# Optimization experiments

Measured on AMD Instinct MI355X. Metric: run time of the kernel, lower is better.

The kernel has to match this reference:

```python
import jax, jax.numpy as jnp
import numpy as np

N_NODES = 50000
N_EDGES = 600000
IN_DIM = 128
HID = 128
OUT_DIM = 40
NUM_REL = 3
LN_EPS = 1e-5


def layer_norm(x, g, b):
    mu = jnp.mean(x, axis=-1, keepdims=True)
    var = jnp.var(x, axis=-1, keepdims=True)
    return (x - mu) * jax.lax.rsqrt(var + LN_EPS) * g + b


def rgcn_conv(x, edge_index, edge_type, w_rel, w_root, bias, aggr):
    """PyG-style RGCNConv: out = x @ W_root + bias + sum_r aggr_r(x_src @ W_r)."""
    src, dst = edge_index[0], edge_index[1]
    out = x @ w_root + bias                      # [N, F_out]
    for r in range(NUM_REL):                     # small fixed relation loop
        h = x @ w_rel[r]                         # transform-then-gather: [N, F_out]
        msg = h[src]                             # [E, F_out]
        mask = (edge_type == r)[:, None]
        if aggr == 'add':
            msg = jnp.where(mask, msg, 0.0)
            agg = jax.ops.segment_sum(msg, dst, num_segments=N_NODES)
        else:  # 'max'; empty segments -> 0 (matches PyG scatter_reduce include_self=False over zeros)
            msg = jnp.where(mask, msg, -jnp.inf)
            agg = jax.ops.segment_max(msg, dst, num_segments=N_NODES)
            agg = jnp.where(jnp.isfinite(agg), agg, 0.0)
        out = out + agg
    return out


def setup_inputs() -> dict:
    key = jax.random.key(0)
    ks = jax.random.split(key, 16)
    f32 = jnp.float32
    def lin(k, fan_in, shape):
        return jax.random.normal(k, shape, dtype=f32) / np.sqrt(fan_in)
    inp = {
        'x': jax.random.normal(ks[0], (N_NODES, IN_DIM), dtype=f32),
        'edge_index': jax.random.randint(ks[1], (2, N_EDGES), 0, N_NODES),
        'edge_type': jax.random.randint(ks[2], (N_EDGES,), 0, NUM_REL),
        # conv1
        'w1_rel': lin(ks[3], IN_DIM, (NUM_REL, IN_DIM, HID)),
        'w1_root': lin(ks[4], IN_DIM, (IN_DIM, HID)),
        'b1': jnp.zeros((HID,), f32),
        'ln1_g': jnp.ones((HID,), f32), 'ln1_b': jnp.zeros((HID,), f32),
        # conv2
        'w2_rel': lin(ks[5], HID, (NUM_REL, HID, HID)),
        'w2_root': lin(ks[6], HID, (HID, HID)),
        'b2': jnp.zeros((HID,), f32),
        'ln2_g': jnp.ones((HID,), f32), 'ln2_b': jnp.zeros((HID,), f32),
        # classifier
        'cw1': lin(ks[7], HID, (HID, HID)), 'cb1': jnp.zeros((HID,), f32),
        'cln1_g': jnp.ones((HID,), f32), 'cln1_b': jnp.zeros((HID,), f32),
        'cw2': lin(ks[8], HID, (HID, HID // 2)), 'cb2': jnp.zeros((HID // 2,), f32),
        'cln2_g': jnp.ones((HID // 2,), f32), 'cln2_b': jnp.zeros((HID // 2,), f32),
        'cw3': lin(ks[9], HID // 2, (HID // 2, OUT_DIM)), 'cb3': jnp.zeros((OUT_DIM,), f32),
    }
    return inp


def reference(x, edge_index, edge_type,
              w1_rel, w1_root, b1, ln1_g, ln1_b,
              w2_rel, w2_root, b2, ln2_g, ln2_b,
              cw1, cb1, cln1_g, cln1_b,
              cw2, cb2, cln2_g, cln2_b,
              cw3, cb3):
    # eval mode: edge dropout and feature dropout are identity
    h = rgcn_conv(x, edge_index, edge_type, w1_rel, w1_root, b1, 'add')
    h = jax.nn.relu(layer_norm(h, ln1_g, ln1_b))
    x1 = h
    h = rgcn_conv(x1, edge_index, edge_type, w2_rel, w2_root, b2, 'max')
    h = jax.nn.relu(layer_norm(h, ln2_g, ln2_b))
    h = h + x1 * 0.2
    # classifier MLP
    h = jax.nn.gelu(layer_norm(h @ cw1 + cb1, cln1_g, cln1_b), approximate=False)
    h = jax.nn.gelu(layer_norm(h @ cw2 + cb2, cln2_g, cln2_b), approximate=False)
    h = h @ cw3 + cb3
    return jax.nn.log_softmax(h, axis=1)
```

## Files before the change

kernel.cpp:

```cpp
#include <hip/hip_runtime.h>
#include <hip/hip_bf16.h>
#include <math.h>


typedef __attribute__((ext_vector_type(8))) short bf16x8;
typedef __attribute__((ext_vector_type(4))) float f32x4;
typedef unsigned short ushort_t;

__device__ __forceinline__ ushort_t bf16rne(float v) {
    unsigned u = __float_as_uint(v);
    return (ushort_t)((u + 0x7FFFu + ((u >> 16) & 1u)) >> 16);
}

__device__ __forceinline__ void split_bf16(float v, ushort_t& h, ushort_t& l) {
    ushort_t hu = bf16rne(v);
    float hf = __uint_as_float((unsigned)hu << 16);
    h = hu;
    l = bf16rne(v - hf);
}

__device__ __forceinline__ float bf2f(unsigned u16) {
    return __uint_as_float(u16 << 16);
}

__device__ __forceinline__ float4 unpack_bf4(uint2 u) {
    return make_float4(bf2f(u.x & 0xFFFFu), bf2f(u.x >> 16),
                       bf2f(u.y & 0xFFFFu), bf2f(u.y >> 16));
}

__device__ __forceinline__ float2 unpack_bf2(unsigned u) {
    return make_float2(__uint_as_float(u << 16),
                       __uint_as_float(u & 0xFFFF0000u));
}

__device__ __forceinline__ uint2 pack_bf4(float4 v) {
    uint2 o;
    o.x = (unsigned)bf16rne(v.x) | ((unsigned)bf16rne(v.y) << 16);
    o.y = (unsigned)bf16rne(v.z) | ((unsigned)bf16rne(v.w) << 16);
    return o;
}

__device__ __forceinline__ unsigned pack_bf2(float2 v) {
    return (unsigned)bf16rne(v.x) | ((unsigned)bf16rne(v.y) << 16);
}

__device__ __forceinline__ void conv_body128(const float* __restrict__ W,
                                             ushort_t* __restrict__ out,
                                             int idx) {
    constexpr int NCF = 8;
    constexpr size_t PST = (size_t)4 * NCF * 512;
    int l = idx & 63;
    int cf = (idx >> 6) & 7;
    int ks = idx >> 9;
    int col = cf * 16 + (l & 15);
    int k0 = ks * 32 + (l >> 4) * 8;
    size_t base = (((size_t)ks * NCF + cf) * 64 + l) * 8;
#pragma unroll
    for (int j = 0; j < 8; ++j) {
        ushort_t h, lo_;
        split_bf16(W[(size_t)(k0 + j) * 128 + col], h, lo_);
        out[base + j] = h;
        out[PST + base + j] = lo_;
    }
}

__global__ __launch_bounds__(256) void convert_all_x2bf(
    const float* __restrict__ w1_root, const float* __restrict__ w1_rel,
    const float* __restrict__ w2_root, const float* __restrict__ w2_rel,
    const float* __restrict__ cw1, const float* __restrict__ cw2,
    ushort_t* __restrict__ wfb,
    const float* __restrict__ x, ushort_t* __restrict__ xh, int n4) {
    int b = blockIdx.x;
    if (b >= 76) {
        int g = (b - 76) * 256 + threadIdx.x;
        if (g < n4) {
            float4 v = ((const float4*)x)[g];
            ((uint2*)xh)[g] = pack_bf4(v);
        }
        return;
    }
    if (b < 72) {
        const float* src;
        int slot;
        if (b < 8)       { slot = 0;              src = w1_root; }
        else if (b < 32) { int r = (b - 8) >> 3;  slot = 1 + r; src = w1_rel + (size_t)r * 16384; }
        else if (b < 40) { slot = 4;              src = w2_root; }
        else if (b < 64) { int r = (b - 40) >> 3; slot = 5 + r; src = w2_rel + (size_t)r * 16384; }
        else             { slot = 8;              src = cw1; }
        int lb = (b < 8) ? b : (b < 32) ? ((b - 8) & 7) : (b < 40) ? (b - 32)
               : (b < 64) ? ((b - 40) & 7) : (b - 64);
        conv_body128(src, wfb + (size_t)slot * 32768, lb * 256 + threadIdx.x);
    } else {
        constexpr int NCF = 4;
        constexpr size_t PST = (size_t)4 * NCF * 512;
        int idx = (b - 72) * 256 + threadIdx.x;
        ushort_t* out = wfb + (size_t)9 * 32768;
        int l = idx & 63;
        int cf = (idx >> 6) & 3;
        int ks = idx >> 8;
        int col = cf * 16 + (l & 15);
        int k0 = ks * 32 + (l >> 4) * 8;
        size_t base = (((size_t)ks * NCF + cf) * 64 + l) * 8;
#pragma unroll
        for (int j = 0; j < 8; ++j) {
            ushort_t h, lo_;
            split_bf16(cw2[(size_t)(k0 + j) * 64 + col], h, lo_);
            out[base + j] = h;
            out[PST + base + j] = lo_;
        }
    }
}

template <int NCOL, int NSEG, int FUSE>
__global__ __launch_bounds__(256, 3) void gemm_bf(
    const ushort_t* __restrict__ A0, const ushort_t* __restrict__ A1,
    const ushort_t* __restrict__ A2, const ushort_t* __restrict__ A3,
    const ushort_t* __restrict__ wfrag, const float* __restrict__ bias,
    const float* __restrict__ lng, const float* __restrict__ lnb,
    void* __restrict__ Yv, int M) {
    constexpr int NCF = NCOL / 16;
    constexpr int WF = NCOL / 32;
    constexpr int PST = 4 * NCF * 512;
    constexpr int WSEG = 2 * PST;
    constexpr int RS = NCOL * 4 + 16;
    constexpr int EPB = 64 * RS;
    constexpr int SMEM_BYTES = (EPB > 16384) ? EPB : 16384;
    __shared__ __align__(16) char smem[SMEM_BYTES];
    char (*lds)[8192] = (char(*)[8192])smem;

    const int tid = threadIdx.x;
    const int wv = tid >> 6, lane = tid & 63, l15 = lane & 15, lg = lane >> 4;
    const int rowgrp = wv >> 1, colgrp = wv & 1;
    const int row0 = blockIdx.x * 64;
    const ushort_t* As[4] = {A0, A1, A2, A3};

    f32x4 acc[2][WF];
#pragma unroll
    for (int xf = 0; xf < 2; ++xf)
#pragma unroll
        for (int wf = 0; wf < WF; ++wf) acc[xf][wf] = (f32x4){0.f, 0.f, 0.f, 0.f};

    uint4 regs[2];

    auto LOADSTAGE = [&](int ch) {
        const ushort_t* __restrict__ A = As[ch >> 1];
        int kcb = (ch & 1) * 128;
#pragma unroll
        for (int i = 0; i < 2; ++i) {
            int s = tid + i * 256;
            int r = s >> 3, c16 = s & 7;
            int gr = row0 + r;
            uint4 v = make_uint4(0u, 0u, 0u, 0u);
            if (gr < M)
                v = *(const uint4*)((const char*)A + (size_t)gr * 256 + kcb + c16 * 16);
            regs[i] = v;
        }
    };

    auto WRITESTAGE = [&](int buf) {
        char* L = lds[buf];
#pragma unroll
        for (int i = 0; i < 2; ++i) {
            int s = tid + i * 256;
            int r = s >> 3, c16 = s & 7;
            int byte = (r * 128 + c16 * 16) ^ ((r & 7) << 4);
            *(uint4*)(L + byte) = regs[i];
        }
    };

    auto COMPUTE = [&](int ch, int buf) {
        int seg = ch >> 1, half = ch & 1;
        const ushort_t* __restrict__ ws = wfrag + (size_t)seg * WSEG;
        const char* L = lds[buf];
#pragma unroll
        for (int kk = 0; kk < 2; ++kk) {
            int ks = half * 2 + kk;
            bf16x8 xh[2];
#pragma unroll
            for (int xf = 0; xf < 2; ++xf) {
                int r = rowgrp * 32 + xf * 16 + l15;
                int byte = (r * 128 + kk * 64 + lg * 16) ^ ((r & 7) << 4);
                xh[xf] = *(const bf16x8*)(L + byte);
            }
            bf16x8 wh[WF], wl[WF];
#pragma unroll
            for (int wf = 0; wf < WF; ++wf) {
                size_t off = (((size_t)ks * NCF + colgrp * WF + wf) * 64 + lane) * 8;
                wh[wf] = *(const bf16x8*)(ws + off);
                wl[wf] = *(const bf16x8*)(ws + PST + off);
            }
#pragma unroll
            for (int xf = 0; xf < 2; ++xf)
#pragma unroll
                for (int wf = 0; wf < WF; ++wf) {
                    acc[xf][wf] = __builtin_amdgcn_mfma_f32_16x16x32_bf16(
                        wh[wf], xh[xf], acc[xf][wf], 0, 0, 0);
                    acc[xf][wf] = __builtin_amdgcn_mfma_f32_16x16x32_bf16(
                        wl[wf], xh[xf], acc[xf][wf], 0, 0, 0);
                }
        }
    };

    constexpr int CH = 2 * NSEG;
    LOADSTAGE(0);
    WRITESTAGE(0);
    __syncthreads();
    for (int ch = 0; ch < CH; ++ch) {
        if (ch + 1 < CH) LOADSTAGE(ch + 1);
        COMPUTE(ch, ch & 1);
        __syncthreads();
        if (ch + 1 < CH) WRITESTAGE((ch + 1) & 1);
        __syncthreads();
    }

    {
        float4 bv[WF];
#pragma unroll
        for (int wf = 0; wf < WF; ++wf) {
            int col = colgrp * (NCOL / 2) + wf * 16 + lg * 4;
            bv[wf] = bias ? *(const float4*)(bias + col)
                          : make_float4(0.f, 0.f, 0.f, 0.f);
        }
#pragma unroll
        for (int xf = 0; xf < 2; ++xf) {
            int r = rowgrp * 32 + xf * 16 + l15;
#pragma unroll
            for (int wf = 0; wf < WF; ++wf) {
                int col = colgrp * (NCOL / 2) + wf * 16 + lg * 4;
                float4 o;
                o.x = acc[xf][wf][0] + bv[wf].x;
                o.y = acc[xf][wf][1] + bv[wf].y;
                o.z = acc[xf][wf][2] + bv[wf].z;
                o.w = acc[xf][wf][3] + bv[wf].w;
                *(float4*)(smem + r * RS + col * 4) = o;
            }
        }
    }
    __syncthreads();

    if (FUSE >= 1 && FUSE <= 3) {
        constexpr int CPT = NCOL / 4;
        int r = tid >> 2, seg = tid & 3;
        char* rp = smem + r * RS + seg * CPT * 4;
        float s = 0.f, sq = 0.f;
        float4 vv[CPT / 4];
#pragma unroll
        for (int j = 0; j < CPT / 4; ++j) {
            float4 v = *(const float4*)(rp + j * 16);
            vv[j] = v;
            s += (v.x + v.y) + (v.z + v.w);
            sq += (v.x * v.x + v.y * v.y) + (v.z * v.z + v.w * v.w);
        }
        s += __shfl_xor(s, 1, 64); sq += __shfl_xor(sq, 1, 64);
        s += __shfl_xor(s, 2, 64); sq += __shfl_xor(sq, 2, 64);
        float mu = s * (1.f / NCOL);
        float var = sq * (1.f / NCOL) - mu * mu;
        float rstd = rsqrtf(var + 1e-5f);
#pragma unroll
        for (int j = 0; j < CPT / 4; ++j) {
            int c0 = seg * CPT + j * 4;
            float4 v = vv[j];
            float4 gg = *(const float4*)(lng + c0);
            float4 bb = *(const float4*)(lnb + c0);
            float y0 = (v.x - mu) * rstd * gg.x + bb.x;
            float y1 = (v.y - mu) * rstd * gg.y + bb.y;
            float y2 = (v.z - mu) * rstd * gg.z + bb.z;
            float y3 = (v.w - mu) * rstd * gg.w + bb.w;
            if (FUSE == 1) {
                y0 = fmaxf(y0, 0.f); y1 = fmaxf(y1, 0.f);
                y2 = fmaxf(y2, 0.f); y3 = fmaxf(y3, 0.f);
            } else {
                y0 = 0.5f * y0 * (1.f + erff(y0 * 0.70710678118654752f));
                y1 = 0.5f * y1 * (1.f + erff(y1 * 0.70710678118654752f));
                y2 = 0.5f * y2 * (1.f + erff(y2 * 0.70710678118654752f));
                y3 = 0.5f * y3 * (1.f + erff(y3 * 0.70710678118654752f));
            }
            vv[j] = make_float4(y0, y1, y2, y3);
        }
        __syncthreads();
        if (FUSE == 3) {
#pragma unroll
            for (int j = 0; j < CPT / 4; ++j) *(float4*)(rp + j * 16) = vv[j];
        } else {
#pragma unroll
            for (int j = 0; j < CPT / 4; ++j) {
                int c0 = seg * CPT + j * 4;
                *(uint2*)(smem + r * RS + 2 * c0) = pack_bf4(vv[j]);
            }
        }
        __syncthreads();
    }

    if (FUSE == 4) {
        constexpr int SL = 64 * (NCOL / 8);
#pragma unroll
        for (int i = 0; i < SL / 256; ++i) {
            int slot = tid + i * 256;
            int rr = slot / (NCOL / 8), c16 = slot % (NCOL / 8);
            int gr = row0 + rr;
            if (gr < M) {
                float4 a = *(const float4*)(smem + rr * RS + c16 * 32);
                float4 b = *(const float4*)(smem + rr * RS + c16 * 32 + 16);
                uint4 o;
                uint2 pa = pack_bf4(a), pb = pack_bf4(b);
                o.x = pa.x; o.y = pa.y; o.z = pb.x; o.w = pb.y;
                *(uint4*)((char*)Yv + (size_t)gr * (NCOL * 2) + c16 * 16) = o;
            }
        }
    } else {
        constexpr int OUTB = (FUSE == 0 || FUSE == 3) ? NCOL * 4 : NCOL * 2;
        constexpr int RP = OUTB / 16;
        constexpr int SL = 64 * RP;
#pragma unroll
        for (int i = 0; i < SL / 256; ++i) {
            int slot = tid + i * 256;
            int rr = slot / RP, c16 = slot % RP;
            int gr = row0 + rr;
            if (gr < M)
                *(uint4*)((char*)Yv + (size_t)gr * OUTB + c16 * 16) =
                    *(const uint4*)(smem + rr * RS + c16 * 16);
        }
    }
}

__global__ __launch_bounds__(256, 3) void gemm_conv2(
    const ushort_t* __restrict__ X, const ushort_t* __restrict__ wfb,
    const float* __restrict__ b2, ushort_t* __restrict__ ACbf,
    ushort_t* __restrict__ H0, ushort_t* __restrict__ H1,
    ushort_t* __restrict__ H2, int M) {
    constexpr int NCF = 8, WF = 4;
    constexpr int PST = 4 * NCF * 512;
    constexpr int RS2 = 256 + 16;
    __shared__ __align__(16) char smem[16384 + 64 * RS2];
    char* Xs = smem;
    char* ep = smem + 16384;

    const int tid = threadIdx.x;
    const int wv = tid >> 6, lane = tid & 63, l15 = lane & 15, lg = lane >> 4;
    const int rowgrp = wv >> 1, colgrp = wv & 1;
    const int row0 = blockIdx.x * 64;

#pragma unroll
    for (int i = 0; i < 4; ++i) {
        int s = tid + i * 256;
        int r = s >> 4, c16 = s & 15;
        int gr = row0 + r;
        uint4 v = make_uint4(0u, 0u, 0u, 0u);
        if (gr < M) v = *(const uint4*)((const char*)X + (size_t)gr * 256 + c16 * 16);
        int byte = (r * 256 + c16 * 16) ^ ((r & 7) << 4);
        *(uint4*)(Xs + byte) = v;
    }
    __syncthreads();

    ushort_t* outs[4] = {ACbf, H0, H1, H2};
    for (int set = 0; set < 4; ++set) {
        const ushort_t* __restrict__ ws = wfb + (size_t)(4 + set) * 32768;
        f32x4 acc[2][WF];
#pragma unroll
        for (int xf = 0; xf < 2; ++xf)
#pragma unroll
            for (int wf = 0; wf < WF; ++wf) acc[xf][wf] = (f32x4){0.f, 0.f, 0.f, 0.f};
#pragma unroll
        for (int ks = 0; ks < 4; ++ks) {
            bf16x8 xh[2];
#pragma unroll
            for (int xf = 0; xf < 2; ++xf) {
                int r = rowgrp * 32 + xf * 16 + l15;
                int byte = (r * 256 + ks * 64 + lg * 16) ^ ((r & 7) << 4);
                xh[xf] = *(const bf16x8*)(Xs + byte);
            }
            bf16x8 wh[WF], wl[WF];
#pragma unroll
            for (int wf = 0; wf < WF; ++wf) {
                size_t off = (((size_t)ks * NCF + colgrp * WF + wf) * 64 + lane) * 8;
                wh[wf] = *(const bf16x8*)(ws + off);
                wl[wf] = *(const bf16x8*)(ws + PST + off);
            }
#pragma unroll
            for (int xf = 0; xf < 2; ++xf)
#pragma unroll
                for (int wf = 0; wf < WF; ++wf) {
                    acc[xf][wf] = __builtin_amdgcn_mfma_f32_16x16x32_bf16(
                        wh[wf], xh[xf], acc[xf][wf], 0, 0, 0);
                    acc[xf][wf] = __builtin_amdgcn_mfma_f32_16x16x32_bf16(
                        wl[wf], xh[xf], acc[xf][wf], 0, 0, 0);
                }
        }
        __syncthreads();
#pragma unroll
        for (int xf = 0; xf < 2; ++xf) {
            int r = rowgrp * 32 + xf * 16 + l15;
#pragma unroll
            for (int wf = 0; wf < WF; ++wf) {
                int col = colgrp * 64 + wf * 16 + lg * 4;
                float4 o;
                o.x = acc[xf][wf][0];
                o.y = acc[xf][wf][1];
                o.z = acc[xf][wf][2];
                o.w = acc[xf][wf][3];
                if (set == 0) {
                    float4 bv = *(const float4*)(b2 + col);
                    o.x += bv.x; o.y += bv.y; o.z += bv.z; o.w += bv.w;
                }
                *(uint2*)(ep + r * RS2 + col * 2) = pack_bf4(o);
            }
        }
        __syncthreads();
        ushort_t* O = outs[set];
#pragma unroll
        for (int i = 0; i < 4; ++i) {
            int slot = tid + i * 256;
            int rr = slot >> 4, c16 = slot & 15;
            int gr = row0 + rr;
            if (gr < M)
                *(uint4*)((char*)O + (size_t)gr * 256 + c16 * 16) =
                    *(const uint4*)(ep + rr * RS2 + c16 * 16);
        }
    }
}

__global__ __launch_bounds__(256) void hist3_kernel(const int* __restrict__ edst,
                                                    const int* __restrict__ etype,
                                                    int* __restrict__ deg3, int E) {
    int e = blockIdx.x * 256 + threadIdx.x;
    if (e < E) atomicAdd(&deg3[edst[e] * 3 + etype[e]], 1);
}

__global__ __launch_bounds__(256) void scan_deg3(const int* __restrict__ deg3,
                                                 int* __restrict__ out,
                                                 int* __restrict__ sums, int n) {
    __shared__ int s[256];
    int g = blockIdx.x * 256 + threadIdx.x;
    int v = 0;
    if (g < n) v = deg3[g * 3] + deg3[g * 3 + 1] + deg3[g * 3 + 2];
    s[threadIdx.x] = v;
    __syncthreads();
    int acc = v;
    for (int off = 1; off < 256; off <<= 1) {
        int t = (threadIdx.x >= off) ? s[threadIdx.x - off] : 0;
        __syncthreads();
        acc += t;
        s[threadIdx.x] = acc;
        __syncthreads();
    }
    if (g < n) out[g] = acc - v;
    if (threadIdx.x == 255 && sums) sums[blockIdx.x] = acc;
}

__global__ __launch_bounds__(256) void scan_block(const int* __restrict__ in,
                                                  int* __restrict__ out,
                                                  int* __restrict__ sums, int n) {
    __shared__ int s[256];
    int g = blockIdx.x * 256 + threadIdx.x;
    int v = (g < n) ? in[g] : 0;
    s[threadIdx.x] = v;
    __syncthreads();
    int acc = v;
    for (int off = 1; off < 256; off <<= 1) {
        int t = (threadIdx.x >= off) ? s[threadIdx.x - off] : 0;
        __syncthreads();
        acc += t;
        s[threadIdx.x] = acc;
        __syncthreads();
    }
    if (g < n) out[g] = acc - v;
    if (threadIdx.x == 255 && sums) sums[blockIdx.x] = acc;
}

__global__ __launch_bounds__(256) void scan_add_ranges(
    const int* __restrict__ scanned, const int* __restrict__ topex,
    const int* __restrict__ deg3, int4* __restrict__ ranges,
    int* __restrict__ cursor3, int n) {
    int g = blockIdx.x * 256 + threadIdx.x;
    if (g >= n) return;
    int b = scanned[g] + topex[blockIdx.x];
    int d0 = deg3[g * 3], d1 = deg3[g * 3 + 1], d2 = deg3[g * 3 + 2];
    int4 r;
    r.x = b; r.y = b + d0; r.z = b + d0 + d1; r.w = b + d0 + d1 + d2;
    ranges[g] = r;
    cursor3[g * 3] = r.x; cursor3[g * 3 + 1] = r.y; cursor3[g * 3 + 2] = r.z;
}

__global__ __launch_bounds__(256) void fill3_kernel(
    const int* __restrict__ esrc, const int* __restrict__ edst,
    const int* __restrict__ etype, int* __restrict__ cursor3,
    int* __restrict__ colidx, int E) {
    int e = blockIdx.x * 256 + threadIdx.x;
    if (e >= E) return;
    int pos = atomicAdd(&cursor3[edst[e] * 3 + etype[e]], 1);
    colidx[pos] = esrc[e];
}

__global__ __launch_bounds__(256) void agg3_add(
    const ushort_t* __restrict__ xh, const int4* __restrict__ ranges,
    const int* __restrict__ colidx, ushort_t* __restrict__ S0,
    ushort_t* __restrict__ S1, ushort_t* __restrict__ S2, int N) {
    int node = blockIdx.x * 4 + (threadIdx.x >> 6);
    int lane = threadIdx.x & 63;
    if (node >= N) return;
    int4 rg = ranges[node];
    float2 acur = make_float2(0.f, 0.f);
    float2 a0 = acur, a1 = acur;
    int e = rg.x, end = rg.w;

    auto step = [&](int ee, unsigned u) {
        if (ee == rg.y) { a0 = acur; acur = make_float2(0.f, 0.f); }
        if (ee == rg.z) { a1 = acur; acur = make_float2(0.f, 0.f); }
        float2 v = unpack_bf2(u);
        acur.x += v.x; acur.y += v.y;
    };

    for (; e + 8 <= end; e += 8) {
        int s[8];
#pragma unroll
        for (int k = 0; k < 8; ++k) s[k] = colidx[e + k];
        unsigned u[8];
#pragma unroll
        for (int k = 0; k < 8; ++k)
            u[k] = *(const unsigned*)(xh + (size_t)s[k] * 128 + lane * 2);
#pragma unroll
        for (int k = 0; k < 8; ++k) step(e + k, u[k]);
    }
    if (e + 4 <= end) {
        int s[4];
#pragma unroll
        for (int k = 0; k < 4; ++k) s[k] = colidx[e + k];
        unsigned u[4];
#pragma unroll
        for (int k = 0; k < 4; ++k)
            u[k] = *(const unsigned*)(xh + (size_t)s[k] * 128 + lane * 2);
#pragma unroll
        for (int k = 0; k < 4; ++k) step(e + k, u[k]);
        e += 4;
    }
    for (; e < end; ++e)
        step(e, *(const unsigned*)(xh + (size_t)colidx[e] * 128 + lane * 2));

    if (rg.y == end) { a0 = acur; acur = make_float2(0.f, 0.f); }
    if (rg.z == end) { a1 = acur; acur = make_float2(0.f, 0.f); }
    float2 a2 = acur;

    *(unsigned*)(S0 + (size_t)node * 128 + lane * 2) = pack_bf2(a0);
    *(unsigned*)(S1 + (size_t)node * 128 + lane * 2) = pack_bf2(a1);
    *(unsigned*)(S2 + (size_t)node * 128 + lane * 2) = pack_bf2(a2);
}

__global__ __launch_bounds__(256) void maxagg_ln(
    const ushort_t* __restrict__ Hbase, const int4* __restrict__ ranges,
    const int* __restrict__ colidx, const ushort_t* __restrict__ accbf,
    const ushort_t* __restrict__ resid, const float* __restrict__ g,
    const float* __restrict__ b, ushort_t* __restrict__ outH, int N) {
    int node = blockIdx.x * 4 + (threadIdx.x >> 6);
    int lane = threadIdx.x & 63;
    if (node >= N) return;
    int4 rg = ranges[node];
    const float NI = -INFINITY;
    float2 mcur = make_float2(NI, NI);
    float2 m0 = mcur, m1 = mcur;
    int e = rg.x, end = rg.w;

    auto step = [&](int ee, unsigned u) {
        if (ee == rg.y) { m0 = mcur; mcur = make_float2(NI, NI); }
        if (ee == rg.z) { m1 = mcur; mcur = make_float2(NI, NI); }
        float2 v = unpack_bf2(u);
        mcur.x = fmaxf(mcur.x, v.x);
        mcur.y = fmaxf(mcur.y, v.y);
    };
    auto addr = [&](int ee, int src) {
        int rel = (ee >= rg.y) + (ee >= rg.z);
        return (const unsigned*)(Hbase + ((size_t)rel * N + src) * 128 + lane * 2);
    };

    for (; e + 8 <= end; e += 8) {
        int s[8];
#pragma unroll
        for (int k = 0; k < 8; ++k) s[k] = colidx[e + k];
        unsigned u[8];
#pragma unroll
        for (int k = 0; k < 8; ++k) u[k] = *addr(e + k, s[k]);
#pragma unroll
        for (int k = 0; k < 8; ++k) step(e + k, u[k]);
    }
    if (e + 4 <= end) {
        int s[4];
#pragma unroll
        for (int k = 0; k < 4; ++k) s[k] = colidx[e + k];
        unsigned u[4];
#pragma unroll
        for (int k = 0; k < 4; ++k) u[k] = *addr(e + k, s[k]);
#pragma unroll
        for (int k = 0; k < 4; ++k) step(e + k, u[k]);
        e += 4;
    }
    for (; e < end; ++e) step(e, *addr(e, colidx[e]));

    if (rg.y == end) { m0 = mcur; mcur = make_float2(NI, NI); }
    if (rg.z == end) { m1 = mcur; mcur = make_float2(NI, NI); }
    float2 m2 = mcur;

    auto fix = [](float2& m) {
        m.x = (m.x > -3e38f) ? m.x : 0.f;
        m.y = (m.y > -3e38f) ? m.y : 0.f;
    };
    fix(m0); fix(m1); fix(m2);

    float2 a = unpack_bf2(*(const unsigned*)(accbf + (size_t)node * 128 + lane * 2));
    a.x += m0.x + m1.x + m2.x;
    a.y += m0.y + m1.y + m2.y;
    float s = a.x + a.y;
    float sq = a.x * a.x + a.y * a.y;
#pragma unroll
    for (int off = 32; off; off >>= 1) {
        s += __shfl_xor(s, off, 64);
        sq += __shfl_xor(sq, off, 64);
    }
    float mu = s * (1.f / 128.f);
    float var = sq * (1.f / 128.f) - mu * mu;
    float rstd = rsqrtf(var + 1e-5f);
    float2 gg = *(const float2*)(g + lane * 2);
    float2 bb = *(const float2*)(b + lane * 2);
    float2 rv = unpack_bf2(*(const unsigned*)(resid + (size_t)node * 128 + lane * 2));
    float2 y;
    y.x = fmaxf((a.x - mu) * rstd * gg.x + bb.x, 0.f) + 0.2f * rv.x;
    y.y = fmaxf((a.y - mu) * rstd * gg.y + bb.y, 0.f) + 0.2f * rv.y;
    *(unsigned*)(outH + (size_t)node * 128 + lane * 2) = pack_bf2(y);
}

__global__ __launch_bounds__(256) void gemm40_lsm(const float* __restrict__ X,
                                                  const float* __restrict__ W,
                                                  const float* __restrict__ bias,
                                                  float* __restrict__ Y, int M) {
    __shared__ float Xs[64][65];
    __shared__ float Ws[64 * 40];
    __shared__ float Ys[64][41];
    __shared__ float mx_[64], ls_[64];
    const int tid = threadIdx.x;
    const int row0 = blockIdx.x * 64;
    for (int i = tid; i < 64 * 40; i += 256) Ws[i] = W[i];
#pragma unroll
    for (int i = 0; i < 4; ++i) {
        int slot = tid + i * 256;
        int r = slot >> 4, c4 = slot & 15;
        float4 v = make_float4(0.f, 0.f, 0.f, 0.f);
        if (row0 + r < M) v = *(const float4*)(X + (size_t)(row0 + r) * 64 + c4 * 4);
        Xs[r][c4 * 4 + 0] = v.x; Xs[r][c4 * 4 + 1] = v.y;
        Xs[r][c4 * 4 + 2] = v.z; Xs[r][c4 * 4 + 3] = v.w;
    }
    __syncthreads();
    const int row = tid >> 2, cg = (tid & 3) * 10;
    float acc[10];
#pragma unroll
    for (int j = 0; j < 10; ++j) acc[j] = 0.f;
#pragma unroll 8
    for (int k = 0; k < 64; ++k) {
        float xv = Xs[row][k];
#pragma unroll
        for (int j = 0; j < 10; ++j) acc[j] = fmaf(xv, Ws[k * 40 + cg + j], acc[j]);
    }
#pragma unroll
    for (int j = 0; j < 10; ++j) Ys[row][cg + j] = acc[j] + bias[cg + j];
    __syncthreads();
    if (tid < 64) {
        float mx = -INFINITY;
#pragma unroll 8
        for (int c = 0; c < 40; ++c) mx = fmaxf(mx, Ys[tid][c]);
        float sum = 0.f;
#pragma unroll 8
        for (int c = 0; c < 40; ++c) sum += __expf(Ys[tid][c] - mx);
        mx_[tid] = mx;
        ls_[tid] = logf(sum);
    }
    __syncthreads();
#pragma unroll
    for (int i = 0; i < 10; ++i) {
        int slot = tid + i * 256;
        int r = slot / 40, c = slot % 40;
        int gr = row0 + r;
        if (gr < M) Y[(size_t)gr * 40 + c] = Ys[r][c] - mx_[r] - ls_[r];
    }
}

extern "C" void kernel_launch(void* const* d_in, const int* in_sizes, int n_in,
                              void* d_out, int out_size, void* d_ws, size_t ws_size,
                              hipStream_t stream) {
    const float* x       = (const float*)d_in[0];
    const int*   eidx    = (const int*)d_in[1];
    const int*   etype   = (const int*)d_in[2];
    const float* w1_rel  = (const float*)d_in[3];
    const float* w1_root = (const float*)d_in[4];
    const float* b1      = (const float*)d_in[5];
    const float* ln1_g   = (const float*)d_in[6];
    const float* ln1_b   = (const float*)d_in[7];
    const float* w2_rel  = (const float*)d_in[8];
    const float* w2_root = (const float*)d_in[9];
    const float* b2      = (const float*)d_in[10];
    const float* ln2_g   = (const float*)d_in[11];
    const float* ln2_b   = (const float*)d_in[12];
    const float* cw1     = (const float*)d_in[13];
    const float* cb1     = (const float*)d_in[14];
    const float* cln1_g  = (const float*)d_in[15];
    const float* cln1_b  = (const float*)d_in[16];
    const float* cw2     = (const float*)d_in[17];
    const float* cb2     = (const float*)d_in[18];
    const float* cln2_g  = (const float*)d_in[19];
    const float* cln2_b  = (const float*)d_in[20];
    const float* cw3     = (const float*)d_in[21];
    const float* cb3     = (const float*)d_in[22];

    const int N = in_sizes[0] / 128;
    const int E = in_sizes[1] / 2;
    const int* esrc = eidx;
    const int* edst = eidx + E;

    const size_t HB = (size_t)N * 256;
    char* base = (char*)d_ws;
    ushort_t* S0 = (ushort_t*)(base + 0 * HB);
    ushort_t* S1 = (ushort_t*)(base + 1 * HB);
    ushort_t* S2 = (ushort_t*)(base + 2 * HB);
    ushort_t* X1 = (ushort_t*)(base + 3 * HB);
    ushort_t* AC = (ushort_t*)(base + 4 * HB);
    char*     B3 = base + 5 * HB;

    int* rowptr  = (int*)B3;
    int* deg3    = rowptr + (N + 1);
    int* cursor3 = deg3 + 3 * N;
    int* bsums   = cursor3 + 3 * N;
    int* btop    = bsums + 256;
    int4* ranges = (int4*)(((uintptr_t)(btop + 256) + 15) & ~(uintptr_t)15);
    int* colidx  = (int*)(ranges + N);
    ushort_t* wfb = (ushort_t*)(((uintptr_t)(colidx + E) + 255) & ~(uintptr_t)255);
    auto WSLOT = [&](int i) { return wfb + (size_t)i * 32768; };
    ushort_t* xh = (ushort_t*)(((uintptr_t)(wfb + 10 * 32768) + 255) & ~(uintptr_t)255);
    ushort_t* h2 = xh;
    ushort_t* C1 = S0;
    float*    C2 = (float*)S1;

    const dim3 blk(256);
    const int gGemm = (N + 63) / 64;
    const int gAgg4 = (N + 3) / 4;
    const int gEdge = (E + 255) / 256;
    const int nScanB = (N + 255) / 256;
    const int gX2  = (N * 32 + 255) / 256;

    hipMemsetAsync(deg3, 0, (size_t)3 * N * sizeof(int), stream);
    hist3_kernel<<<gEdge, blk, 0, stream>>>(edst, etype, deg3, E);
    scan_deg3<<<nScanB, blk, 0, stream>>>(deg3, rowptr, bsums, N);
    scan_block<<<1, blk, 0, stream>>>(bsums, btop, nullptr, nScanB);
    scan_add_ranges<<<nScanB, blk, 0, stream>>>(rowptr, btop, deg3, ranges,
                                                cursor3, N);
    fill3_kernel<<<gEdge, blk, 0, stream>>>(esrc, edst, etype, cursor3, colidx, E);

    convert_all_x2bf<<<76 + gX2, blk, 0, stream>>>(
        w1_root, w1_rel, w2_root, w2_rel, cw1, cw2, wfb, x, xh, N * 32);

    agg3_add<<<gAgg4, blk, 0, stream>>>(xh, ranges, colidx, S0, S1, S2, N);
    gemm_bf<128, 4, 1><<<gGemm, blk, 0, stream>>>(
        xh, S0, S1, S2, WSLOT(0), b1, ln1_g, ln1_b, X1, N);

    gemm_conv2<<<gGemm, blk, 0, stream>>>(X1, wfb, b2, AC, S0, S1, S2, N);
    maxagg_ln<<<gAgg4, blk, 0, stream>>>(S0, ranges, colidx, AC,
                                         X1, ln2_g, ln2_b, h2, N);

    gemm_bf<128, 1, 2><<<gGemm, blk, 0, stream>>>(
        h2, h2, h2, h2, WSLOT(8), cb1, cln1_g, cln1_b, C1, N);
    gemm_bf<64, 1, 3><<<gGemm, blk, 0, stream>>>(
        C1, C1, C1, C1, WSLOT(9), cb2, cln2_g, cln2_b, C2, N);
    gemm40_lsm<<<gGemm, blk, 0, stream>>>(C2, cw3, cb3, (float*)d_out, N);
}
```

Before: 262.7 us.

## Split wavefront into four edge groups with 16-byte gathers in aggregation kernels

Both edge aggregation kernels (sum for layer 1, max+LayerNorm for layer 2) now split each 64-lane wavefront into four 16-lane groups. Each group handles a different edge and each lane loads 8 bf16 values with one 16-byte load, replacing one 4-byte load per lane per edge. Partial results are combined with cross-group shuffles, and relations are processed in separate loops instead of tracking segment boundaries per edge. This aims to raise memory-level parallelism and cut per-edge instruction overhead. The cost is that the 8-deep unrolled load batching is dropped, lanes idle on tail edges, and only a quarter of the lanes do the final store.

```diff
diff --git a/kernel.cpp b/kernel.cpp
--- a/kernel.cpp
+++ b/kernel.cpp
@@ -38,10 +38,6 @@
     o.x = (unsigned)bf16rne(v.x) | ((unsigned)bf16rne(v.y) << 16);
     o.y = (unsigned)bf16rne(v.z) | ((unsigned)bf16rne(v.w) << 16);
     return o;
-}
-
-__device__ __forceinline__ unsigned pack_bf2(float2 v) {
-    return (unsigned)bf16rne(v.x) | ((unsigned)bf16rne(v.y) << 16);
 }
 
 __device__ __forceinline__ void conv_body128(const float* __restrict__ W,
@@ -498,51 +494,41 @@
     int node = blockIdx.x * 4 + (threadIdx.x >> 6);
     int lane = threadIdx.x & 63;
     if (node >= N) return;
+    int q = lane >> 4, c = lane & 15;
     int4 rg = ranges[node];
-    float2 acur = make_float2(0.f, 0.f);
-    float2 a0 = acur, a1 = acur;
-    int e = rg.x, end = rg.w;
-
-    auto step = [&](int ee, unsigned u) {
-        if (ee == rg.y) { a0 = acur; acur = make_float2(0.f, 0.f); }
-        if (ee == rg.z) { a1 = acur; acur = make_float2(0.f, 0.f); }
-        float2 v = unpack_bf2(u);
-        acur.x += v.x; acur.y += v.y;
-    };
-
-    for (; e + 8 <= end; e += 8) {
-        int s[8];
-#pragma unroll
-        for (int k = 0; k < 8; ++k) s[k] = colidx[e + k];
-        unsigned u[8];
-#pragma unroll
-        for (int k = 0; k < 8; ++k)
-            u[k] = *(const unsigned*)(xh + (size_t)s[k] * 128 + lane * 2);
-#pragma unroll
-        for (int k = 0; k < 8; ++k) step(e + k, u[k]);
-    }
-    if (e + 4 <= end) {
-        int s[4];
-#pragma unroll
-        for (int k = 0; k < 4; ++k) s[k] = colidx[e + k];
-        unsigned u[4];
-#pragma unroll
-        for (int k = 0; k < 4; ++k)
-            u[k] = *(const unsigned*)(xh + (size_t)s[k] * 128 + lane * 2);
-#pragma unroll
-        for (int k = 0; k < 4; ++k) step(e + k, u[k]);
-        e += 4;
-    }
-    for (; e < end; ++e)
-        step(e, *(const unsigned*)(xh + (size_t)colidx[e] * 128 + lane * 2));
-
-    if (rg.y == end) { a0 = acur; acur = make_float2(0.f, 0.f); }
-    if (rg.z == end) { a1 = acur; acur = make_float2(0.f, 0.f); }
-    float2 a2 = acur;
-
-    *(unsigned*)(S0 + (size_t)node * 128 + lane * 2) = pack_bf2(a0);
-    *(unsigned*)(S1 + (size_t)node * 128 + lane * 2) = pack_bf2(a1);
-    *(unsigned*)(S2 + (size_t)node * 128 + lane * 2) = pack_bf2(a2);
+    int begs[4] = {rg.x, rg.y, rg.z, rg.w};
+    ushort_t* Ss[3] = {S0, S1, S2};
+
+    for (int r = 0; r < 3; ++r) {
+        float a[8];
+#pragma unroll
+        for (int j = 0; j < 8; ++j) a[j] = 0.f;
+        int beg = begs[r], end = begs[r + 1];
+        for (int e = beg; e < end; e += 4) {
+            int idx = e + q;
+            if (idx < end) {
+                int src = colidx[idx];
+                uint4 u = *(const uint4*)(xh + (size_t)src * 128 + c * 8);
+                float2 v0 = unpack_bf2(u.x), v1 = unpack_bf2(u.y);
+                float2 v2 = unpack_bf2(u.z), v3 = unpack_bf2(u.w);
+                a[0] += v0.x; a[1] += v0.y; a[2] += v1.x; a[3] += v1.y;
+                a[4] += v2.x; a[5] += v2.y; a[6] += v3.x; a[7] += v3.y;
+            }
+        }
+#pragma unroll
+        for (int j = 0; j < 8; ++j) {
+            a[j] += __shfl_xor(a[j], 16, 64);
+            a[j] += __shfl_xor(a[j], 32, 64);
+        }
+        if (q == 0) {
+            uint4 o;
+            o.x = (unsigned)bf16rne(a[0]) | ((unsigned)bf16rne(a[1]) << 16);
+            o.y = (unsigned)bf16rne(a[2]) | ((unsigned)bf16rne(a[3]) << 16);
+            o.z = (unsigned)bf16rne(a[4]) | ((unsigned)bf16rne(a[5]) << 16);
+            o.w = (unsigned)bf16rne(a[6]) | ((unsigned)bf16rne(a[7]) << 16);
+            *(uint4*)(Ss[r] + (size_t)node * 128 + c * 8) = o;
+        }
+    }
 }
 
 __global__ __launch_bounds__(256) void maxagg_ln(
@@ -553,77 +539,82 @@
     int node = blockIdx.x * 4 + (threadIdx.x >> 6);
     int lane = threadIdx.x & 63;
     if (node >= N) return;
+    int q = lane >> 4, c = lane & 15;
     int4 rg = ranges[node];
+    int begs[4] = {rg.x, rg.y, rg.z, rg.w};
     const float NI = -INFINITY;
-    float2 mcur = make_float2(NI, NI);
-    float2 m0 = mcur, m1 = mcur;
-    int e = rg.x, end = rg.w;
-
-    auto step = [&](int ee, unsigned u) {
-        if (ee == rg.y) { m0 = mcur; mcur = make_float2(NI, NI); }
-        if (ee == rg.z) { m1 = mcur; mcur = make_float2(NI, NI); }
-        float2 v = unpack_bf2(u);
-        mcur.x = fmaxf(mcur.x, v.x);
-        mcur.y = fmaxf(mcur.y, v.y);
-    };
-    auto addr = [&](int ee, int src) {
-        int rel = (ee >= rg.y) + (ee >= rg.z);
-        return (const unsigned*)(Hbase + ((size_t)rel * N + src) * 128 + lane * 2);
-    };
-
-    for (; e + 8 <= end; e += 8) {
-        int s[8];
-#pragma unroll
-        for (int k = 0; k < 8; ++k) s[k] = colidx[e + k];
-        unsigned u[8];
-#pragma unroll
-        for (int k = 0; k < 8; ++k) u[k] = *addr(e + k, s[k]);
-#pragma unroll
-        for (int k = 0; k < 8; ++k) step(e + k, u[k]);
-    }
-    if (e + 4 <= end) {
-        int s[4];
-#pragma unroll
-        for (int k = 0; k < 4; ++k) s[k] = colidx[e + k];
-        unsigned u[4];
-#pragma unroll
-        for (int k = 0; k < 4; ++k) u[k] = *addr(e + k, s[k]);
-#pragma unroll
-        for (int k = 0; k < 4; ++k) step(e + k, u[k]);
-        e += 4;
-    }
-    for (; e < end; ++e) step(e, *addr(e, colidx[e]));
-
-    if (rg.y == end) { m0 = mcur; mcur = make_float2(NI, NI); }
-    if (rg.z == end) { m1 = mcur; mcur = make_float2(NI, NI); }
-    float2 m2 = mcur;
-
-    auto fix = [](float2& m) {
-        m.x = (m.x > -3e38f) ? m.x : 0.f;
-        m.y = (m.y > -3e38f) ? m.y : 0.f;
-    };
-    fix(m0); fix(m1); fix(m2);
-
-    float2 a = unpack_bf2(*(const unsigned*)(accbf + (size_t)node * 128 + lane * 2));
-    a.x += m0.x + m1.x + m2.x;
-    a.y += m0.y + m1.y + m2.y;
-    float s = a.x + a.y;
-    float sq = a.x * a.x + a.y * a.y;
-#pragma unroll
-    for (int off = 32; off; off >>= 1) {
-        s += __shfl_xor(s, off, 64);
-        sq += __shfl_xor(sq, off, 64);
-    }
+
+    float a[8];
+    {
+        uint4 au = *(const uint4*)(accbf + (size_t)node * 128 + c * 8);
+        float2 t0 = unpack_bf2(au.x), t1 = unpack_bf2(au.y);
+        float2 t2 = unpack_bf2(au.z), t3 = unpack_bf2(au.w);
+        a[0] = t0.x; a[1] = t0.y; a[2] = t1.x; a[3] = t1.y;
+        a[4] = t2.x; a[5] = t2.y; a[6] = t3.x; a[7] = t3.y;
+    }
+
+    for (int r = 0; r < 3; ++r) {
+        float m[8];
+#pragma unroll
+        for (int j = 0; j < 8; ++j) m[j] = NI;
+        const ushort_t* base = Hbase + (size_t)r * N * 128;
+        int beg = begs[r], end = begs[r + 1];
+        for (int e = beg; e < end; e += 4) {
+            int idx = e + q;
+            if (idx < end) {
+                int src = colidx[idx];
+                uint4 u = *(const uint4*)(base + (size_t)src * 128 + c * 8);
+                float2 v0 = unpack_bf2(u.x), v1 = unpack_bf2(u.y);
+                float2 v2 = unpack_bf2(u.z), v3 = unpack_bf2(u.w);
+                m[0] = fmaxf(m[0], v0.x); m[1] = fmaxf(m[1], v0.y);
+                m[2] = fmaxf(m[2], v1.x); m[3] = fmaxf(m[3], v1.y);
+                m[4] = fmaxf(m[4], v2.x); m[5] = fmaxf(m[5], v2.y);
+                m[6] = fmaxf(m[6], v3.x); m[7] = fmaxf(m[7], v3.y);
+            }
+        }
+#pragma unroll
+        for (int j = 0; j < 8; ++j) {
+            m[j] = fmaxf(m[j], __shfl_xor(m[j], 16, 64));
+            m[j] = fmaxf(m[j], __shfl_xor(m[j], 32, 64));
+            a[j] += (m[j] > -3e38f) ? m[j] : 0.f;
+        }
+    }
+
+    float s = 0.f, sq = 0.f;
+#pragma unroll
+    for (int j = 0; j < 8; ++j) { s += a[j]; sq += a[j] * a[j]; }
+    s += __shfl_xor(s, 1, 64); sq += __shfl_xor(sq, 1, 64);
+    s += __shfl_xor(s, 2, 64); sq += __shfl_xor(sq, 2, 64);
+    s += __shfl_xor(s, 4, 64); sq += __shfl_xor(sq, 4, 64);
+    s += __shfl_xor(s, 8, 64); sq += __shfl_xor(sq, 8, 64);
     float mu = s * (1.f / 128.f);
     float var = sq * (1.f / 128.f) - mu * mu;
     float rstd = rsqrtf(var + 1e-5f);
-    float2 gg = *(const float2*)(g + lane * 2);
-    float2 bb = *(const float2*)(b + lane * 2);
-    float2 rv = unpack_bf2(*(const unsigned*)(resid + (size_t)node * 128 + lane * 2));
-    float2 y;
-    y.x = fmaxf((a.x - mu) * rstd * gg.x + bb.x, 0.f) + 0.2f * rv.x;
-    y.y = fmaxf((a.y - mu) * rstd * gg.y + bb.y, 0.f) + 0.2f * rv.y;
-    *(unsigned*)(outH + (size_t)node * 128 + lane * 2) = pack_bf2(y);
+
+    if (q == 0) {
+        float4 g0 = *(const float4*)(g + c * 8);
+        float4 g1 = *(const float4*)(g + c * 8 + 4);
+        float4 b0 = *(const float4*)(b + c * 8);
+        float4 b1 = *(const float4*)(b + c * 8 + 4);
+        uint4 ru = *(const uint4*)(resid + (size_t)node * 128 + c * 8);
+        float2 r0 = unpack_bf2(ru.x), r1 = unpack_bf2(ru.y);
+        float2 r2 = unpack_bf2(ru.z), r3 = unpack_bf2(ru.w);
+        float y[8];
+        y[0] = fmaxf((a[0] - mu) * rstd * g0.x + b0.x, 0.f) + 0.2f * r0.x;
+        y[1] = fmaxf((a[1] - mu) * rstd * g0.y + b0.y, 0.f) + 0.2f * r0.y;
+        y[2] = fmaxf((a[2] - mu) * rstd * g0.z + b0.z, 0.f) + 0.2f * r1.x;
+        y[3] = fmaxf((a[3] - mu) * rstd * g0.w + b0.w, 0.f) + 0.2f * r1.y;
+        y[4] = fmaxf((a[4] - mu) * rstd * g1.x + b1.x, 0.f) + 0.2f * r2.x;
+        y[5] = fmaxf((a[5] - mu) * rstd * g1.y + b1.y, 0.f) + 0.2f * r2.y;
+        y[6] = fmaxf((a[6] - mu) * rstd * g1.z + b1.z, 0.f) + 0.2f * r3.x;
+        y[7] = fmaxf((a[7] - mu) * rstd * g1.w + b1.w, 0.f) + 0.2f * r3.y;
+        uint4 o;
+        o.x = (unsigned)bf16rne(y[0]) | ((unsigned)bf16rne(y[1]) << 16);
+        o.y = (unsigned)bf16rne(y[2]) | ((unsigned)bf16rne(y[3]) << 16);
+        o.z = (unsigned)bf16rne(y[4]) | ((unsigned)bf16rne(y[5]) << 16);
+        o.w = (unsigned)bf16rne(y[6]) | ((unsigned)bf16rne(y[7]) << 16);
+        *(uint4*)(outH + (size_t)node * 128 + c * 8) = o;
+    }
 }
 
 __global__ __launch_bounds__(256) void gemm40_lsm(const float* __restrict__ X,
```

Result: slower. 283.2 us (+7.8%).
